# Kernel optimization log

Measured on AMD Instinct MI355X. Metric: run time of the kernel, lower is better.

The kernel has to match this reference:

```python
import jax, jax.numpy as jnp
import numpy as np

STRIDES = (4, 8, 16, 32, 64)
RATIOS = (0.5, 1.0, 2.0)
SCALE = 8.0
A = 3
PRE_NMS = 2000
MAX_PER_IMG = 1000
NMS_THR = 0.7
MAX_RATIO = float(abs(np.log(16.0 / 1000.0)))  # wh_ratio_clip = 16/1000
LEVEL_OFFSET = 4096.0  # > max image coordinate, separates levels for batched NMS
FEAT_HW = ((208, 336), (104, 168), (52, 84), (26, 42), (13, 21))
N = 8


def grid_anchors(stride, H, W):
    # mmdet-style base anchors: scale 8, ratios (0.5,1,2), centered at 0
    r = jnp.asarray(RATIOS, jnp.float32)
    h_r = jnp.sqrt(r)
    w_r = 1.0 / h_r
    ws = stride * w_r * SCALE
    hs = stride * h_r * SCALE
    base = jnp.stack([-ws / 2, -hs / 2, ws / 2, hs / 2], axis=-1)  # [A,4]
    sx = jnp.arange(W, dtype=jnp.float32) * stride
    sy = jnp.arange(H, dtype=jnp.float32) * stride
    yy, xx = jnp.meshgrid(sy, sx, indexing='ij')
    shifts = jnp.stack([xx, yy, xx, yy], axis=-1).reshape(-1, 4)  # [H*W,4], row-major
    return (shifts[:, None, :] + base[None, :, :]).reshape(-1, 4)  # [H*W*A,4]


def decode(anchors, deltas, h, w):
    # DeltaXYWH decode with means 0, stds 1, clip to image
    px = (anchors[..., 0] + anchors[..., 2]) * 0.5
    py = (anchors[..., 1] + anchors[..., 3]) * 0.5
    pw = anchors[..., 2] - anchors[..., 0]
    ph = anchors[..., 3] - anchors[..., 1]
    dx, dy = deltas[..., 0], deltas[..., 1]
    dw = jnp.clip(deltas[..., 2], -MAX_RATIO, MAX_RATIO)
    dh = jnp.clip(deltas[..., 3], -MAX_RATIO, MAX_RATIO)
    gx = px + pw * dx
    gy = py + ph * dy
    gw = pw * jnp.exp(dw)
    gh = ph * jnp.exp(dh)
    x1 = jnp.clip(gx - gw * 0.5, 0.0, w)
    y1 = jnp.clip(gy - gh * 0.5, 0.0, h)
    x2 = jnp.clip(gx + gw * 0.5, 0.0, w)
    y2 = jnp.clip(gy + gh * 0.5, 0.0, h)
    return jnp.stack([x1, y1, x2, y2], axis=-1)


def iou_matrix(b):
    area = (b[:, 2] - b[:, 0]) * (b[:, 3] - b[:, 1])
    lt = jnp.maximum(b[:, None, :2], b[None, :, :2])
    rb = jnp.minimum(b[:, None, 2:], b[None, :, 2:])
    wh = jnp.clip(rb - lt, 0.0, None)
    inter = wh[..., 0] * wh[..., 1]
    union = area[:, None] + area[None, :] - inter
    return inter / jnp.maximum(union, 1e-6)


def _forward(cls_list, reg_list, image_h, image_w):
    scores_all, deltas_all, anchors_all, levels_all = [], [], [], []
    for lvl, (cls, reg) in enumerate(zip(cls_list, reg_list)):
        n, _, H, W = cls.shape
        anchors = grid_anchors(STRIDES[lvl], H, W)  # [H*W*A,4]
        s = jax.nn.sigmoid(jnp.transpose(cls, (0, 2, 3, 1)).reshape(n, -1))
        d = jnp.transpose(reg, (0, 2, 3, 1)).reshape(n, -1, 4)
        k = min(PRE_NMS, s.shape[1])  # topk pre-selection per level
        sv, si = jax.lax.top_k(s, k)
        dv = jnp.take_along_axis(d, si[..., None], axis=1)
        av = anchors[si]
        scores_all.append(sv)
        deltas_all.append(dv)
        anchors_all.append(av)
        levels_all.append(jnp.full((k,), lvl, jnp.int32))
    scores = jnp.concatenate(scores_all, axis=1)    # [N,M]
    deltas = jnp.concatenate(deltas_all, axis=1)    # [N,M,4]
    anchors = jnp.concatenate(anchors_all, axis=1)  # [N,M,4]
    levels = jnp.concatenate(levels_all)            # [M] (same per image)
    boxes = decode(anchors, deltas, float(image_h), float(image_w))
    # filter_boxes with min_area = prod((0,0)) = 0: keep boxes with area >= 0
    area = (boxes[..., 2] - boxes[..., 0]) * (boxes[..., 3] - boxes[..., 1])
    scores = jnp.where(area >= 0.0, scores, -1.0)
    M = boxes.shape[1]
    idxs = jnp.arange(M)

    def nms_one(bs):
        b_i, s_i = bs
        order = jnp.argsort(-s_i)
        b = b_i[order]
        s = s_i[order]
        lv = levels[order]
        # batched NMS: offset each level so cross-level boxes never overlap
        ob = jax.lax.stop_gradient(b + (lv.astype(b.dtype) * LEVEL_OFFSET)[:, None])
        iou = iou_matrix(ob)  # [M,M]

        def body(i, keep):
            sup = (iou[i] > NMS_THR) & (idxs > i) & keep[i]
            return keep & (~sup)

        keep = jax.lax.fori_loop(0, M, body, jnp.ones((M,), bool))
        rank = jnp.cumsum(keep.astype(jnp.int32)) - 1
        tgt = jnp.where(keep & (rank < MAX_PER_IMG), rank, MAX_PER_IMG)  # dump slot
        out_b = jnp.zeros((MAX_PER_IMG + 1, 4), b.dtype).at[tgt].set(b)[:MAX_PER_IMG]
        out_s = jnp.zeros((MAX_PER_IMG + 1,), s.dtype).at[tgt].set(s)[:MAX_PER_IMG]
        return out_b, out_s

    pb, ps = jax.lax.map(nms_one, (boxes, scores))  # sequential per image
    return pb, ps  # [N,1000,4], [N,1000] (zero-padded)


def setup_inputs() -> dict:
    key = jax.random.key(0)
    inp = {}
    for lvl, (H, W) in enumerate(FEAT_HW):
        k1 = jax.random.fold_in(key, 2 * lvl)
        k2 = jax.random.fold_in(key, 2 * lvl + 1)
        inp[f"class_out_{lvl}"] = jax.random.normal(k1, (N, A, H, W), jnp.float32)
        inp[f"reg_out_{lvl}"] = jax.random.normal(k2, (N, 4 * A, H, W), jnp.float32)
    inp["image_h"] = 832
    inp["image_w"] = 1344
    return inp


def reference(class_out_0, class_out_1, class_out_2, class_out_3, class_out_4,
              reg_out_0, reg_out_1, reg_out_2, reg_out_3, reg_out_4,
              image_h, image_w):
    cls_list = [class_out_0, class_out_1, class_out_2, class_out_3, class_out_4]
    reg_list = [reg_out_0, reg_out_1, reg_out_2, reg_out_3, reg_out_4]
    return _forward(cls_list, reg_list, image_h, image_w)
```

## Files before the change

kernel.cpp:

```cpp
#include <hip/hip_runtime.h>
#include <cmath>

#pragma clang fp contract(off)

namespace {
constexpr int NIMG = 8;
constexpr int NLVL = 5;
constexpr int LH[5]   = {208,104,52,26,13};
constexpr int LW[5]   = {336,168,84,42,21};
constexpr int LSTR[5] = {4,8,16,32,64};
constexpr int HWA[5]  = {209664,52416,13104,3276,819};
constexpr int KSEL[5] = {2000,2000,2000,2000,819};
constexpr int SOFF[5] = {0,2000,4000,6000,8000};
constexpr int MTOT    = 8819;
constexpr int CAP     = 6144;
constexpr int NPAIR   = NIMG*NLVL;
constexpr int CCUM[5] = {52,65,69,70,71};
constexpr int BLK_PER_IMG = 71;
constexpr int MASK_W  = 32;
constexpr int OUTK    = 1000;
constexpr int NT2[5]  = {272,272,272,272,55};

constexpr size_t OFF_HIST   = 0;
constexpr size_t OFF_PKC    = 0;
constexpr size_t OFF_CNT    = 655360;
constexpr size_t OFF_RNK    = 655872;
constexpr size_t ZERO_BYTES = 1638912;
constexpr size_t OFF_SELKEY = 1921120;
constexpr size_t OFF_SELBOX = 2767744;
constexpr size_t OFF_MASK   = 3896576;
constexpr size_t OFF_CKEY   = OFF_MASK;
constexpr size_t OFF_CBOX   = OFF_MASK + 2097152;
constexpr size_t OFF_KEEP   = 24376576;
}

struct Ins {
  const float* cls[5];
  const float* reg[5];
  const int* ih;
  const int* iw;
};

__device__ __forceinline__ void decode_block(int b, int& img, int& lvl, int& chunk) {
  img = b / BLK_PER_IMG;
  int rb = b - img*BLK_PER_IMG;
  if      (rb < CCUM[0]) { lvl=0; chunk=rb; }
  else if (rb < CCUM[1]) { lvl=1; chunk=rb-CCUM[0]; }
  else if (rb < CCUM[2]) { lvl=2; chunk=rb-CCUM[1]; }
  else if (rb < CCUM[3]) { lvl=3; chunk=rb-CCUM[2]; }
  else                   { lvl=4; chunk=0; }
}

__device__ __forceinline__ unsigned mapbits(float x) {
  unsigned u = __float_as_uint(x);
  return u ^ (unsigned)(((int)u >> 31) | (int)0x80000000);
}

__device__ __forceinline__ float sigmoid_ref(float x) {
  float e = (float)exp(-(double)x);
  return 1.0f / (1.0f + e);
}

__global__ void k_hist(Ins in, unsigned* __restrict__ hist, float4* __restrict__ outz) {
  {
    const int NOUT = NIMG*OUTK*5*4/16;
    float4 z = make_float4(0.f,0.f,0.f,0.f);
    int i0 = blockIdx.x*256 + threadIdx.x, stride = gridDim.x*256;
    for (int j = i0; j < NOUT; j += stride) outz[j] = z;
  }
  int img, lvl, chunk; decode_block(blockIdx.x, img, lvl, chunk);
  __shared__ unsigned lh[4096];
  for (int i = threadIdx.x; i < 4096; i += 256) lh[i] = 0;
  __syncthreads();
  const float* src = in.cls[lvl] + (size_t)img * HWA[lvl];
  if (lvl != 4) {
    const float4* src4 = (const float4*)src;
    int nf4 = HWA[lvl] >> 2;
    int base4 = chunk * 1024;
    #pragma unroll
    for (int j = 0; j < 4; j++) {
      int f = base4 + j*256 + threadIdx.x;
      if (f < nf4) {
        float4 v = src4[f];
        atomicAdd(&lh[mapbits(v.x) >> 20], 1u);
        atomicAdd(&lh[mapbits(v.y) >> 20], 1u);
        atomicAdd(&lh[mapbits(v.z) >> 20], 1u);
        atomicAdd(&lh[mapbits(v.w) >> 20], 1u);
      }
    }
  } else {
    int base = chunk * 4096;
    #pragma unroll
    for (int j = 0; j < 16; j++) {
      int e = base + j*256 + threadIdx.x;
      if (e < HWA[4]) atomicAdd(&lh[mapbits(src[e]) >> 20], 1u);
    }
  }
  __syncthreads();
  unsigned* gh = hist + (img*NLVL + lvl) * 4096;
  for (int i = threadIdx.x; i < 4096; i += 256)
    if (lh[i]) atomicAdd(&gh[i], lh[i]);
}

__global__ void __launch_bounds__(256) k_compact(Ins in, const unsigned* __restrict__ hist,
                          unsigned* __restrict__ cnt,
                          unsigned long long* __restrict__ ckey,
                          float4* __restrict__ cbox) {
  int img, lvl, chunk; decode_block(blockIdx.x, img, lvl, chunk);
  int pair = img*NLVL + lvl;
  __shared__ unsigned part[256];
  __shared__ unsigned sT;
  const unsigned* gh = hist + (size_t)pair * 4096;
  {
    unsigned s = 0;
    #pragma unroll
    for (int i = 0; i < 16; i++) s += gh[threadIdx.x*16 + i];
    part[threadIdx.x] = s;
  }
  __syncthreads();
  if (threadIdx.x == 0) {
    unsigned k = (unsigned)KSEL[lvl];
    unsigned cum = 0, T = 0;
    for (int t = 255; t >= 0; t--) {
      if (cum + part[t] >= k) {
        unsigned edge = 0;
        for (int b = t*16 + 15; b >= t*16; b--) {
          cum += gh[b];
          if (cum >= k) { edge = (unsigned)b; break; }
        }
        T = edge << 20;
        break;
      }
      cum += part[t];
    }
    sT = T;
  }
  __syncthreads();
  unsigned T = sT;

  const float* src = in.cls[lvl] + (size_t)img * HWA[lvl];
  int hw = LH[lvl] * LW[lvl];
  int lid = threadIdx.x & 63;
  __shared__ unsigned lbuf[4096];
  __shared__ unsigned long long lkey[4096];
  __shared__ unsigned lc, gbase;
  if (threadIdx.x == 0) lc = 0;
  __syncthreads();

  auto emit = [&](int e, float v, bool sel) {
    unsigned long long mask = __ballot(sel);
    if (mask != 0ull) {
      int leader = __ffsll((long long)mask) - 1;
      unsigned wb = 0;
      if (lid == leader) wb = atomicAdd(&lc, (unsigned)__popcll(mask));
      wb = (unsigned)__shfl((int)wb, leader, 64);
      if (sel) {
        unsigned p = wb + (unsigned)__popcll(mask & ((1ull << lid) - 1ull));
        int a = e / hw;
        int r = e - a*hw;
        unsigned idx = (unsigned)(r*3 + a);
        lbuf[p] = idx;
        float s = sigmoid_ref(v);
        unsigned pack = ((unsigned)lvl << 18) | idx;
        lkey[p] = ((unsigned long long)__float_as_uint(s) << 21)
                | (unsigned long long)(0x1FFFFFu - pack);
      }
    }
  };

  if (lvl != 4) {
    const float4* src4 = (const float4*)src;
    int nf4 = HWA[lvl] >> 2;
    int base4 = chunk * 1024;
    #pragma unroll
    for (int j = 0; j < 4; j++) {
      int f = base4 + j*256 + threadIdx.x;
      bool inb = f < nf4;
      float4 v4 = make_float4(0.f, 0.f, 0.f, 0.f);
      if (inb) v4 = src4[f];
      int e0 = f * 4;
      emit(e0+0, v4.x, inb && (mapbits(v4.x) >= T));
      emit(e0+1, v4.y, inb && (mapbits(v4.y) >= T));
      emit(e0+2, v4.z, inb && (mapbits(v4.z) >= T));
      emit(e0+3, v4.w, inb && (mapbits(v4.w) >= T));
    }
  } else {
    int base = chunk * 4096;
    #pragma unroll
    for (int j = 0; j < 16; j++) {
      int e = base + j*256 + threadIdx.x;
      float v = 0.0f;
      bool inb = (e < HWA[4]);
      if (inb) v = src[e];
      emit(e, v, inb && (mapbits(v) >= T));
    }
  }
  __syncthreads();
  if (threadIdx.x == 0) gbase = atomicAdd(&cnt[pair], lc);
  __syncthreads();
  unsigned nsel = lc, gb = gbase;
  float Wi = (float)(*in.iw), Hi = (float)(*in.ih);
  int Wl = LW[lvl];
  float st = (float)LSTR[lvl];
  const float* rg = in.reg[lvl] + (size_t)img * 4 * HWA[lvl];
  for (unsigned t = threadIdx.x; t < nsel; t += 256) {
    unsigned p = gb + t;
    if (p < CAP) {
      unsigned idx = lbuf[t];
      ckey[(size_t)pair*CAP + p] = lkey[t];
      int a = (int)(idx % 3u);
      int r = (int)(idx / 3u);
      int x = r % Wl, y = r / Wl;
      float dx = rg[(a*4+0)*hw + r];
      float dy = rg[(a*4+1)*hw + r];
      float dwv = rg[(a*4+2)*hw + r];
      float dhv = rg[(a*4+3)*hw + r];
      float ratio = (a==0) ? 0.5f : (a==1) ? 1.0f : 2.0f;
      float hr = sqrtf(ratio);
      float wr = 1.0f / hr;
      float wsz = st * wr * 8.0f;
      float hsz = st * hr * 8.0f;
      float xs = (float)x * st, ys = (float)y * st;
      float x1 = xs - wsz*0.5f, x2 = xs + wsz*0.5f;
      float y1 = ys - hsz*0.5f, y2 = ys + hsz*0.5f;
      float px = (x1 + x2) * 0.5f, py = (y1 + y2) * 0.5f;
      float pw = x2 - x1,          ph = y2 - y1;
      const float MR = 4.135166556742356f;
      dwv = fminf(fmaxf(dwv, -MR), MR);
      dhv = fminf(fmaxf(dhv, -MR), MR);
      float gx = px + pw*dx, gy = py + ph*dy;
      float gw = pw * (float)exp((double)dwv);
      float gh2 = ph * (float)exp((double)dhv);
      float4 bb;
      bb.x = fminf(fmaxf(gx - gw*0.5f, 0.0f), Wi);
      bb.y = fminf(fmaxf(gy - gh2*0.5f, 0.0f), Hi);
      bb.z = fminf(fmaxf(gx + gw*0.5f, 0.0f), Wi);
      bb.w = fminf(fmaxf(gy + gh2*0.5f, 0.0f), Hi);
      cbox[(size_t)pair*CAP + p] = bb;
    }
  }
}

__global__ void __launch_bounds__(256) k_racc(const unsigned* __restrict__ cntA,
                       const unsigned long long* __restrict__ ckey,
                       unsigned* __restrict__ rnk) {
  int pair = blockIdx.z;
  int c = min((int)cntA[pair], CAP);
  int tile = blockIdx.x, slice = blockIdx.y;
  if (tile*256 >= c || slice*256 >= c) return;
  const unsigned long long* kp = ckey + (size_t)pair*CAP;
  __shared__ unsigned long long sk[256];
  int g = slice*256 + threadIdx.x;
  sk[threadIdx.x] = (g < c) ? kp[g] : 0ull;
  __syncthreads();
  int jj = tile*256 + threadIdx.x;
  unsigned long long mykey = kp[min(jj, c-1)];
  const ulonglong2* sk2 = (const ulonglong2*)sk;
  int r0 = 0, r1 = 0, r2 = 0, r3 = 0;
  #pragma unroll 8
  for (int j2 = 0; j2 < 128; j2 += 2) {
    ulonglong2 a = sk2[j2];
    ulonglong2 b = sk2[j2+1];
    r0 += (a.x > mykey) ? 1 : 0;
    r1 += (a.y > mykey) ? 1 : 0;
    r2 += (b.x > mykey) ? 1 : 0;
    r3 += (b.y > mykey) ? 1 : 0;
  }
  int rk = (r0 + r1) + (r2 + r3);
  if (jj < c && rk) atomicAdd(&rnk[pair*CAP + jj], (unsigned)rk);
}

__global__ void __launch_bounds__(256) k_rsel(const unsigned* __restrict__ cntA,
                       const unsigned long long* __restrict__ ckey,
                       const float4* __restrict__ cbox,
                       const unsigned* __restrict__ rnk,
                       unsigned long long* __restrict__ sel_key,
                       float* __restrict__ sel_box) {
  int pair = blockIdx.y; int tile = blockIdx.x;
  int img = pair / NLVL, lvl = pair % NLVL;
  int c = min((int)cntA[pair], CAP);
  int jj = tile*256 + threadIdx.x;
  if (jj >= c) return;
  int rk = (int)rnk[pair*CAP + jj];
  if (rk < KSEL[lvl]) {
    int slot = img*MTOT + SOFF[lvl] + rk;
    sel_key[slot] = ckey[(size_t)pair*CAP + jj];
    ((float4*)sel_box)[slot] = cbox[(size_t)pair*CAP + jj];
  }
}

__global__ void __launch_bounds__(256) k_masks(const float* __restrict__ sel_box,
                        unsigned long long* __restrict__ maskbuf) {
  int pair = blockIdx.y; int lvl = pair % NLVL; int img = pair / NLVL;
  int n = KSEL[lvl];
  int nw = (n + 63) >> 6;
  int nwc2 = (nw + 1) >> 1;
  int wv = threadIdx.x >> 6;
  int lane = threadIdx.x & 63;
  int t = blockIdx.x * 4 + wv;
  if (t >= NT2[lvl]) return;
  int rb = 0, cum = 0;
  while (cum + (nwc2 - (rb >> 1)) <= t) { cum += nwc2 - (rb >> 1); rb++; }
  int jw2 = (rb >> 1) + (t - cum);
  int jw0 = 2*jw2, jw1 = jw0 + 1;
  const float4* boxes = ((const float4*)sel_box) + img*MTOT + SOFF[lvl];
  float off = (float)lvl * 4096.0f;
  int c0 = jw0*64 + lane, c1 = c0 + 64;
  float b0x,b0y,b0z,b0w,a0, b1x,b1y,b1z,b1w,a1;
  if (c0 < n) {
    float4 b = boxes[c0];
    b0x = b.x + off; b0y = b.y + off; b0z = b.z + off; b0w = b.w + off;
    a0 = (b0z - b0x) * (b0w - b0y);
  } else { b0x=b0y=b0z=b0w=3.0e8f; a0=0.0f; }
  if (c1 < n) {
    float4 b = boxes[c1];
    b1x = b.x + off; b1y = b.y + off; b1z = b.z + off; b1w = b.w + off;
    a1 = (b1z - b1x) * (b1w - b1y);
  } else { b1x=b1y=b1z=b1w=3.0e8f; a1=0.0f; }
  __shared__ float4 sbox[4][64];
  __shared__ float  sarea[4][64];
  int row0 = rb*64;
  {
    float4 bi0 = boxes[min(row0 + lane, n-1)];
    bi0.x += off; bi0.y += off; bi0.z += off; bi0.w += off;
    sbox[wv][lane] = bi0;
    sarea[wv][lane] = (bi0.z - bi0.x) * (bi0.w - bi0.y);
  }
  bool z0 = (jw0 < rb);
  bool d0 = (jw0 == rb), d1 = (jw1 == rb);
  const float CHI = 0x1.66666ap-1f;
  const float CLO = 0x1.666664p-1f;
  unsigned long long acc0 = 0ull, acc1 = 0ull, unc = 0ull;
  #pragma unroll 16
  for (int r = 0; r < 64; r++) {
    float4 bi = sbox[wv][r];
    float ai = sarea[wv][r];
    float xx1 = fmaxf(bi.x, b0x), yy1 = fmaxf(bi.y, b0y);
    float xx2 = fminf(bi.z, b0z), yy2 = fminf(bi.w, b0w);
    float iw_ = fmaxf(xx2 - xx1, 0.0f), ih_ = fmaxf(yy2 - yy1, 0.0f);
    float in0 = iw_ * ih_;
    float u0 = fmaxf((ai + a0) - in0, 1e-6f);
    float xc1 = fmaxf(bi.x, b1x), yc1 = fmaxf(bi.y, b1y);
    float xc2 = fminf(bi.z, b1z), yc2 = fminf(bi.w, b1w);
    float jw_ = fmaxf(xc2 - xc1, 0.0f), jh_ = fmaxf(yc2 - yc1, 0.0f);
    float in1 = jw_ * jh_;
    float u1 = fmaxf((ai + a1) - in1, 1e-6f);
    unsigned long long h0 = __ballot(in0 >= CHI * u0);
    unsigned long long l0 = __ballot(in0 >= CLO * u0);
    unsigned long long h1 = __ballot(in1 >= CHI * u1);
    unsigned long long l1 = __ballot(in1 >= CLO * u1);
    unc |= (h0 ^ l0) | (h1 ^ l1);
    unsigned long long dm = ~((2ull << r) - 1ull);
    unsigned long long m0 = z0 ? 0ull : (d0 ? (h0 & dm) : h0);
    unsigned long long m1 = d1 ? (h1 & dm) : h1;
    if (lane == r) { acc0 = m0; acc1 = m1; }
  }
  if (unc) {
    const double Md = 0.70000001788139343261718750;
    acc0 = 0ull; acc1 = 0ull;
    #pragma unroll 1
    for (int r = 0; r < 64; r++) {
      float4 bi = sbox[wv][r];
      float ai = sarea[wv][r];
      float xx1 = fmaxf(bi.x, b0x), yy1 = fmaxf(bi.y, b0y);
      float xx2 = fminf(bi.z, b0z), yy2 = fminf(bi.w, b0w);
      float iw_ = fmaxf(xx2 - xx1, 0.0f), ih_ = fmaxf(yy2 - yy1, 0.0f);
      float in0 = iw_ * ih_;
      float u0 = fmaxf((ai + a0) - in0, 1e-6f);
      float xc1 = fmaxf(bi.x, b1x), yc1 = fmaxf(bi.y, b1y);
      float xc2 = fminf(bi.z, b1z), yc2 = fminf(bi.w, b1w);
      float jw_ = fmaxf(xc2 - xc1, 0.0f), jh_ = fmaxf(yc2 - yc1, 0.0f);
      float in1 = jw_ * jh_;
      float u1 = fmaxf((ai + a1) - in1, 1e-6f);
      unsigned long long w0 = __ballot((double)in0 >= Md * (double)u0);
      unsigned long long w1 = __ballot((double)in1 >= Md * (double)u1);
      unsigned long long dm = ~((2ull << r) - 1ull);
      unsigned long long m0 = z0 ? 0ull : (d0 ? (w0 & dm) : w0);
      unsigned long long m1 = d1 ? (w1 & dm) : w1;
      if (lane == r) { acc0 = m0; acc1 = m1; }
    }
  }
  int row = row0 + lane;
  if (row < n) {
    unsigned long long* dst = maskbuf + (size_t)pair*2000*MASK_W + (size_t)row*MASK_W + jw0;
    if (z0) {
      dst[1] = acc1;
    } else {
      ulonglong2 v; v.x = acc0; v.y = acc1;
      *((ulonglong2*)dst) = v;
    }
  }
}

__global__ void __launch_bounds__(1024) k_nms(const unsigned long long* __restrict__ maskbuf,
                      unsigned long long* __restrict__ keep, int* __restrict__ pkc) {
  int pair = blockIdx.x; int lvl = pair % NLVL;
  int n = KSEL[lvl];
  int nw = (n + 63) >> 6;
  const unsigned long long* mrow = maskbuf + (size_t)pair*2000*MASK_W;
  int tid = threadIdx.x;
  int w  = tid & 31;
  int rg = tid >> 5;
  __shared__ unsigned long long rem[32];
  __shared__ unsigned long long diag[64];
  __shared__ unsigned long long skw[32];
  __shared__ unsigned long long sSk;
  __shared__ int lcnt[64];
  if (tid < 32) { rem[tid] = 0ull; skw[tid] = 0ull; }
  __syncthreads();

  unsigned long long A0, A1, B0, B1;
  {
    int r0 = min(rg*2, n-1), r1 = min(rg*2+1, n-1);
    A0 = mrow[(size_t)r0*MASK_W + w];
    A1 = mrow[(size_t)r1*MASK_W + w];
  }
  for (int k = 0; k < nw; k++) {
    if (k + 1 < nw) {
      int r0 = min(64*(k+1) + rg*2, n-1), r1 = min(64*(k+1) + rg*2 + 1, n-1);
      B0 = mrow[(size_t)r0*MASK_W + w];
      B1 = mrow[(size_t)r1*MASK_W + w];
    }
    if (w == k) { diag[rg*2] = A0; diag[rg*2+1] = A1; }
    __syncthreads();
    if (tid < 64) {
      int row = 64*k + tid;
      bool valid = row < n;
      unsigned long long D = valid ? diag[tid] : 0ull;
      unsigned long long rk = rem[k];
      unsigned long long S = rk;
      for (int it = 0; it < 64; it++) {
        bool kept = valid && !((S >> tid) & 1ull);
        unsigned long long c = kept ? D : 0ull;
        #pragma unroll
        for (int m = 1; m < 64; m <<= 1) {
          unsigned lo = (unsigned)__shfl_xor((int)(unsigned)(c & 0xffffffffull), m, 64);
          unsigned hi = (unsigned)__shfl_xor((int)(unsigned)(c >> 32), m, 64);
          c |= ((unsigned long long)hi << 32) | (unsigned long long)lo;
        }
        unsigned long long Snew = rk | c;
        if (Snew == S) break;
        S = Snew;
      }
      if (tid == 0) {
        sSk = S;
        int nb = n - 64*k;
        unsigned long long vm = (nb >= 64) ? ~0ull : ((1ull << nb) - 1ull);
        unsigned long long kw = (~S) & vm;
        skw[k] = kw;
        keep[(size_t)pair*MASK_W + k] = kw;
      }
    }
    __syncthreads();
    if (w > k) {
      unsigned long long Sk = sSk;
      int r0 = 64*k + rg*2, r1 = r0 + 1;
      unsigned long long m = 0ull;
      if (r0 < n && !((Sk >> (rg*2)) & 1ull))     m |= A0;
      if (r1 < n && !((Sk >> (rg*2+1)) & 1ull))   m |= A1;
      if (m) atomicOr(&rem[w], m);
    }
    __syncthreads();
    A0 = B0; A1 = B1;
  }
  if (tid < 64) {
    int lane = tid;
    unsigned long long kw = (lane < nw) ? skw[lane] : 0ull;
    lcnt[lane] = __popcll(kw);
    int pre = 0;
    for (int t2 = 0; t2 < lane; t2++) pre += lcnt[t2];
    for (int b = 0; b < 64; b++) {
      int p = lane*64 + b;
      if (p < n) {
        pre += (int)((kw >> b) & 1ull);
        pkc[pair*2048 + p] = pre;
      }
    }
  }
}

__global__ void __launch_bounds__(256) k_out2(const unsigned long long* __restrict__ sel_key,
                      const float* __restrict__ sel_box,
                      const unsigned long long* __restrict__ keep,
                      const int* __restrict__ pkc,
                      float* __restrict__ out) {
  int img = blockIdx.y;
  int pos = blockIdx.x*256 + threadIdx.x;
  if (pos >= MTOT) return;
  int lvl = pos<2000?0 : pos<4000?1 : pos<6000?2 : pos<8000?3 : 4;
  int local = pos - SOFF[lvl];
  int pair = img*NLVL + lvl;
  unsigned long long kw = keep[(size_t)pair*MASK_W + (local >> 6)];
  if (!((kw >> (local & 63)) & 1ull)) return;
  unsigned long long mykey = sel_key[img*MTOT + pos];
  int rank = pkc[pair*2048 + local] - 1;
  #pragma unroll
  for (int l2 = 0; l2 < NLVL; l2++) {
    if (l2 == lvl) continue;
    const unsigned long long* A = sel_key + img*MTOT + SOFF[l2];
    int lo = 0, hi = KSEL[l2];
    while (lo < hi) {
      int mid = (lo + hi) >> 1;
      if (A[mid] > mykey) lo = mid + 1; else hi = mid;
    }
    if (lo > 0) rank += pkc[(img*NLVL + l2)*2048 + lo - 1];
  }
  if (rank < OUTK) {
    ((float4*)out)[img*OUTK + rank] = ((const float4*)sel_box)[img*MTOT + pos];
    out[NIMG*OUTK*4 + img*OUTK + rank] = __uint_as_float((unsigned)(mykey >> 21));
  }
}

extern "C" void kernel_launch(void* const* d_in, const int* in_sizes, int n_in,
                              void* d_out, int out_size, void* d_ws, size_t ws_size,
                              hipStream_t stream) {
  Ins in;
  for (int l = 0; l < 5; l++) {
    in.cls[l] = (const float*)d_in[2*l];
    in.reg[l] = (const float*)d_in[2*l + 1];
  }
  in.ih = (const int*)d_in[10];
  in.iw = (const int*)d_in[11];

  char* ws = (char*)d_ws;
  unsigned* hist              = (unsigned*)(ws + OFF_HIST);
  int* pkc                    = (int*)(ws + OFF_PKC);
  unsigned* cnt               = (unsigned*)(ws + OFF_CNT);
  unsigned* rnk               = (unsigned*)(ws + OFF_RNK);
  unsigned long long* sel_key = (unsigned long long*)(ws + OFF_SELKEY);
  float* sel_box              = (float*)(ws + OFF_SELBOX);
  unsigned long long* maskbuf = (unsigned long long*)(ws + OFF_MASK);
  unsigned long long* ckey    = (unsigned long long*)(ws + OFF_CKEY);
  float4* cbox                = (float4*)(ws + OFF_CBOX);
  unsigned long long* keep    = (unsigned long long*)(ws + OFF_KEEP);
  float* out                  = (float*)d_out;

  hipMemsetAsync(d_ws, 0, ZERO_BYTES, stream);
  k_hist   <<<NIMG*BLK_PER_IMG, 256, 0, stream>>>(in, hist, (float4*)out);
  k_compact<<<NIMG*BLK_PER_IMG, 256, 0, stream>>>(in, hist, cnt, ckey, cbox);
  k_racc   <<<dim3(CAP/256, CAP/256, NPAIR), 256, 0, stream>>>(cnt, ckey, rnk);
  k_rsel   <<<dim3(CAP/256, NPAIR), 256, 0, stream>>>(cnt, ckey, cbox, rnk, sel_key, sel_box);
  k_masks  <<<dim3(68, NPAIR), 256, 0, stream>>>(sel_box, maskbuf);
  k_nms    <<<NPAIR, 1024, 0, stream>>>(maskbuf, keep, pkc);
  k_out2   <<<dim3((MTOT + 255)/256, NIMG), 256, 0, stream>>>(sel_key, sel_box, keep, pkc, out);
}
```

Baseline: 248.3 us.

## Replace pairwise rank counting with per-pair shared-memory bitonic sort

```diff
diff --git a/kernel.cpp b/kernel.cpp
--- a/kernel.cpp
+++ b/kernel.cpp
@@ -14,6 +14,7 @@
 constexpr int SOFF[5] = {0,2000,4000,6000,8000};
 constexpr int MTOT    = 8819;
 constexpr int CAP     = 6144;
+constexpr int SORTN   = 4096;
 constexpr int NPAIR   = NIMG*NLVL;
 constexpr int CCUM[5] = {52,65,69,70,71};
 constexpr int BLK_PER_IMG = 71;
@@ -24,8 +25,7 @@
 constexpr size_t OFF_HIST   = 0;
 constexpr size_t OFF_PKC    = 0;
 constexpr size_t OFF_CNT    = 655360;
-constexpr size_t OFF_RNK    = 655872;
-constexpr size_t ZERO_BYTES = 1638912;
+constexpr size_t ZERO_BYTES = 655520;
 constexpr size_t OFF_SELKEY = 1921120;
 constexpr size_t OFF_SELBOX = 2767744;
 constexpr size_t OFF_MASK   = 3896576;
@@ -241,51 +241,43 @@
   }
 }
 
-__global__ void __launch_bounds__(256) k_racc(const unsigned* __restrict__ cntA,
-                       const unsigned long long* __restrict__ ckey,
-                       unsigned* __restrict__ rnk) {
-  int pair = blockIdx.z;
-  int c = min((int)cntA[pair], CAP);
-  int tile = blockIdx.x, slice = blockIdx.y;
-  if (tile*256 >= c || slice*256 >= c) return;
-  const unsigned long long* kp = ckey + (size_t)pair*CAP;
-  __shared__ unsigned long long sk[256];
-  int g = slice*256 + threadIdx.x;
-  sk[threadIdx.x] = (g < c) ? kp[g] : 0ull;
-  __syncthreads();
-  int jj = tile*256 + threadIdx.x;
-  unsigned long long mykey = kp[min(jj, c-1)];
-  const ulonglong2* sk2 = (const ulonglong2*)sk;
-  int r0 = 0, r1 = 0, r2 = 0, r3 = 0;
-  #pragma unroll 8
-  for (int j2 = 0; j2 < 128; j2 += 2) {
-    ulonglong2 a = sk2[j2];
-    ulonglong2 b = sk2[j2+1];
-    r0 += (a.x > mykey) ? 1 : 0;
-    r1 += (a.y > mykey) ? 1 : 0;
-    r2 += (b.x > mykey) ? 1 : 0;
-    r3 += (b.y > mykey) ? 1 : 0;
-  }
-  int rk = (r0 + r1) + (r2 + r3);
-  if (jj < c && rk) atomicAdd(&rnk[pair*CAP + jj], (unsigned)rk);
-}
-
-__global__ void __launch_bounds__(256) k_rsel(const unsigned* __restrict__ cntA,
+__global__ void __launch_bounds__(512) k_sort(const unsigned* __restrict__ cntA,
                        const unsigned long long* __restrict__ ckey,
                        const float4* __restrict__ cbox,
-                       const unsigned* __restrict__ rnk,
                        unsigned long long* __restrict__ sel_key,
                        float* __restrict__ sel_box) {
-  int pair = blockIdx.y; int tile = blockIdx.x;
+  int pair = blockIdx.x;
   int img = pair / NLVL, lvl = pair % NLVL;
   int c = min((int)cntA[pair], CAP);
-  int jj = tile*256 + threadIdx.x;
-  if (jj >= c) return;
-  int rk = (int)rnk[pair*CAP + jj];
-  if (rk < KSEL[lvl]) {
-    int slot = img*MTOT + SOFF[lvl] + rk;
-    sel_key[slot] = ckey[(size_t)pair*CAP + jj];
-    ((float4*)sel_box)[slot] = cbox[(size_t)pair*CAP + jj];
+  const unsigned long long* kp = ckey + (size_t)pair*CAP;
+  __shared__ unsigned long long skey[SORTN];
+  __shared__ unsigned sidx[SORTN];
+  for (int i = threadIdx.x; i < SORTN; i += 512) {
+    skey[i] = (i < c) ? kp[i] : 0ull;
+    sidx[i] = (unsigned)i;
+  }
+  for (int k = 2; k <= SORTN; k <<= 1) {
+    for (int j = k >> 1; j > 0; j >>= 1) {
+      __syncthreads();
+      for (int i = threadIdx.x; i < SORTN; i += 512) {
+        int ixj = i ^ j;
+        if (ixj > i) {
+          unsigned long long a = skey[i], b = skey[ixj];
+          bool up = (i & k) == 0;
+          if (up ? (a < b) : (a > b)) {
+            skey[i] = b; skey[ixj] = a;
+            unsigned ta = sidx[i]; sidx[i] = sidx[ixj]; sidx[ixj] = ta;
+          }
+        }
+      }
+    }
+  }
+  __syncthreads();
+  int ks = KSEL[lvl];
+  for (int i = threadIdx.x; i < ks; i += 512) {
+    int slot = img*MTOT + SOFF[lvl] + i;
+    sel_key[slot] = skey[i];
+    ((float4*)sel_box)[slot] = cbox[(size_t)pair*CAP + sidx[i]];
   }
 }
 
@@ -526,7 +518,6 @@
   unsigned* hist              = (unsigned*)(ws + OFF_HIST);
   int* pkc                    = (int*)(ws + OFF_PKC);
   unsigned* cnt               = (unsigned*)(ws + OFF_CNT);
-  unsigned* rnk               = (unsigned*)(ws + OFF_RNK);
   unsigned long long* sel_key = (unsigned long long*)(ws + OFF_SELKEY);
   float* sel_box              = (float*)(ws + OFF_SELBOX);
   unsigned long long* maskbuf = (unsigned long long*)(ws + OFF_MASK);
@@ -538,8 +529,7 @@
   hipMemsetAsync(d_ws, 0, ZERO_BYTES, stream);
   k_hist   <<<NIMG*BLK_PER_IMG, 256, 0, stream>>>(in, hist, (float4*)out);
   k_compact<<<NIMG*BLK_PER_IMG, 256, 0, stream>>>(in, hist, cnt, ckey, cbox);
-  k_racc   <<<dim3(CAP/256, CAP/256, NPAIR), 256, 0, stream>>>(cnt, ckey, rnk);
-  k_rsel   <<<dim3(CAP/256, NPAIR), 256, 0, stream>>>(cnt, ckey, cbox, rnk, sel_key, sel_box);
+  k_sort   <<<NPAIR, 512, 0, stream>>>(cnt, ckey, cbox, sel_key, sel_box);
   k_masks  <<<dim3(68, NPAIR), 256, 0, stream>>>(sel_box, maskbuf);
   k_nms    <<<NPAIR, 1024, 0, stream>>>(maskbuf, keep, pkc);
   k_out2   <<<dim3((MTOT + 255)/256, NIMG), 256, 0, stream>>>(sel_key, sel_box, keep, pkc, out);
```

Result: slower. 329.4 us (+32.7%).
